# Performance work log

Measured on AMD Instinct MI355X. Metric: run time of the kernel, lower is better.

## Reference

```python
import jax, jax.numpy as jnp
import numpy as np


def _solve(f, lmbda, nu, repeats, l):
    h, w, nc = f.shape
    proj = l * (l + 1) // 2
    # enumeration order of (k1,k2) pairs matches the torch double loop
    k1s = np.array([k1 for k1 in range(l) for k2 in range(k1, l)], dtype=np.int32)
    k2s = np.array([k2 for k1 in range(l) for k2 in range(k1, l)], dtype=np.int32)
    zs = np.arange(l)
    # M[p, z] = 1 iff k1s[p] <= z <= k2s[p]  (the k_indices membership)
    M = jnp.asarray(((k1s[:, None] <= zs[None, :]) & (zs[None, :] <= k2s[:, None])).astype(np.float32))
    k1s_j = jnp.asarray(k1s)
    k2s_j = jnp.asarray(k2s)

    sigmap = 1.0 / (3.0 + l)
    sigmas = 1.0
    tauu = 1.0 / 6.0
    tau_mu = 1.0 / (2.0 + proj / 4.0)

    kl = jnp.arange(1, l + 1, dtype=jnp.float32) / l            # k/l, k=1..l
    dist2 = (kl[None, None, None, :] - f[..., None]) ** 2       # (h,w,nc,l)

    def bound(x1, x2):
        return 0.25 * (x1 * x1 + x2 * x2) - lmbda * dist2

    def parabola(p1, p2, p3, ubar, mu1, mu2):
        # forward differences, zero-padded at the far edge
        u1 = jnp.diff(ubar, axis=0, append=ubar[-1:, :, :, :])
        u2 = jnp.diff(ubar, axis=1, append=ubar[:, -1:, :, :])
        u3 = jnp.diff(ubar, axis=3, append=ubar[:, :, :, -1:])
        mu1sum = jnp.einsum('hwcp,pz->hwcz', mu1, M)
        mu2sum = jnp.einsum('hwcp,pz->hwcz', mu2, M)
        u1 = p1 + sigmap * (u1 + mu1sum)
        u2 = p2 + sigmap * (u2 + mu2sum)
        u3 = p3 + sigmap * u3
        B = bound(u1, u2)
        mask = u3 < B
        y = u3 + lmbda * dist2
        norm = jnp.sqrt(u1 * u1 + u2 * u2)
        a = 0.5 * norm                      # 2*0.25*norm
        b = (2.0 / 3.0) * (1.0 - 0.5 * y)   # 2/3*(1 - 2*0.25*y)
        neg_b = b < 0
        sb = jnp.sqrt(jnp.where(neg_b, -b, 1.0))   # sqrt(-b), guarded
        sb3 = sb * sb * sb
        d = jnp.where(neg_b, (a - sb3) * (a + sb3), a * a + b * b * b)
        d_pos = d >= 0
        c = jnp.cbrt(a + jnp.sqrt(jnp.where(d_pos, d, 0.0)))  # a+sqrt(d)>=0
        c_safe = jnp.where(c == 0, 1.0, c)
        ratio = jnp.clip(a / jnp.where(neg_b, sb3, 1.0), -1.0, 1.0)
        v_trig = 2.0 * sb * jnp.cos(jnp.arccos(ratio) / 3.0)
        v = jnp.where(d_pos & (c == 0), 0.0,
                      jnp.where(~d_pos, v_trig, c - b / c_safe))
        norm_safe = jnp.where(norm == 0, 1.0, norm)
        scale = (v / 0.5) / norm_safe       # v/(2*0.25)/norm
        p1n = jnp.where(mask, jnp.where(norm == 0, 0.0, scale * u1), u1)
        p2n = jnp.where(mask, jnp.where(norm == 0, 0.0, scale * u2), u2)
        p3n = jnp.where(mask, bound(p1n, p2n), u3)
        return p1n, p2n, p3n

    def l2proj(s1, s2, mb1, mb2):
        m1 = s1 - sigmas * mb1
        m2 = s2 - sigmas * mb2
        norm = jnp.sqrt(m1 * m1 + m2 * m2)
        mask = norm > nu
        ns = jnp.where(mask, norm, 1.0)
        return jnp.where(mask, m1 * nu / ns, m1), jnp.where(mask, m2 * nu / ns, m2)

    def mu_step(p1, p2, s1, s2, mu1, mu2):
        # interval sums sum_{k=k1..k2} p via exclusive cumsum differences
        zpad = jnp.zeros(p1.shape[:3] + (1,), p1.dtype)
        cs1 = jnp.concatenate([zpad, jnp.cumsum(p1, axis=3)], axis=3)
        cs2 = jnp.concatenate([zpad, jnp.cumsum(p2, axis=3)], axis=3)
        t1 = cs1[..., k2s_j + 1] - cs1[..., k1s_j]
        t2 = cs2[..., k2s_j + 1] - cs2[..., k1s_j]
        mu1n = mu1 + tau_mu * (s1 - t1)
        mu2n = mu2 + tau_mu * (s2 - t2)
        return mu1n, mu2n, 2.0 * mu1n - mu1, 2.0 * mu2n - mu2

    def clipping(p1, p2, p3, u):
        # adjoint (backward) differences of p[:-1] zero-padded on both sides
        z0 = jnp.zeros((1, w, nc, l), u.dtype)
        z1 = jnp.zeros((h, 1, nc, l), u.dtype)
        z3 = jnp.zeros((h, w, nc, 1), u.dtype)
        d1 = jnp.diff(jnp.concatenate([z0, p1[:-1], z0], axis=0), axis=0)
        d2 = jnp.diff(jnp.concatenate([z1, p2[:, :-1], z1], axis=1), axis=1)
        d3 = jnp.diff(jnp.concatenate([z3, p3[..., :-1], z3], axis=3), axis=3)
        un = jnp.clip(u + tauu * (d1 + d2 + d3), 0.0, 1.0)
        un = un.at[..., 0].set(1.0).at[..., l - 1].set(0.0)
        return un, 2.0 * un - u

    u0 = jnp.broadcast_to(f[..., None], (h, w, nc, l)).astype(jnp.float32)
    zl = jnp.zeros((h, w, nc, l), jnp.float32)
    zp = jnp.zeros((h, w, nc, proj), jnp.float32)
    state = (u0, u0, zl, zl, zl, zp, zp, zp, zp, zp, zp, jnp.array(False))

    def body(state, i):
        u, ubar, p1, p2, p3, s1, s2, mu1, mu2, mb1, mb2, done = state
        p1n, p2n, p3n = parabola(p1, p2, p3, ubar, mu1, mu2)
        s1n, s2n = l2proj(s1, s2, mb1, mb2)
        mu1n, mu2n, mb1n, mb2n = mu_step(p1n, p2n, s1n, s2n, mu1, mu2)
        un, ubarn = clipping(p1n, p2n, p3n, u)
        nrj = jnp.sum(jnp.abs(un - u))  # h_u vs h_un
        conv = ((i % 10) == 0) & (nrj / (w * h * l) <= 5e-5)
        keep = lambda old, new: jnp.where(done, old, new)
        new = (keep(u, un), keep(ubar, ubarn), keep(p1, p1n), keep(p2, p2n),
               keep(p3, p3n), keep(s1, s1n), keep(s2, s2n), keep(mu1, mu1n),
               keep(mu2, mu2n), keep(mb1, mb1n), keep(mb2, mb2n), done | conv)
        return new, None

    state, _ = jax.lax.scan(body, state, jnp.arange(repeats))
    return state[0]


def setup_inputs() -> dict:
    key = jax.random.key(0)
    f = jax.random.uniform(key, (384, 384, 1), dtype=jnp.float32)
    return {"f": f, "lmbda": jnp.float32(1.0), "nu": jnp.float32(1.0),
            "repeats": 6, "l": 12}


def reference(f, lmbda, nu, repeats, l):
    return _solve(f, lmbda, nu, repeats, l)
```

## Files before the change

kernel.cpp:

```cpp
#include <hip/hip_runtime.h>
#include <hip/hip_fp16.h>
#include <math.h>

#define H 384
#define W 384
#define NPIX (H * W)
#define L 12
#define REPEATS 6
#define LNP ((size_t)L * NPIX)

__host__ __device__ constexpr int pbase(int k1) { return k1 * L - (k1 * (k1 - 1)) / 2; }

struct alignas(8) P1 { __half2 mu, d; };

__device__ __forceinline__ void parabola_proj(float u1, float u2, float u3, float ld2,
                                              float& p1n, float& p2n, float& p3n) {
  const float n2 = u1 * u1 + u2 * u2;
  const float Bb = 0.25f * n2 - ld2;
  const bool mask = u3 < Bb;
  const float y = u3 + ld2;
  const float norm = sqrtf(n2);
  const float a = 0.5f * norm;
  const float b = (2.0f / 3.0f) * (1.0f - 0.5f * y);
  const bool neg_b = b < 0.0f;
  const float sb = sqrtf(neg_b ? -b : 1.0f);
  const float sb3 = sb * sb * sb;
  const float d = neg_b ? (a - sb3) * (a + sb3) : (a * a + b * b * b);
  const bool d_pos = d >= 0.0f;
  const float c = cbrtf(a + sqrtf(d_pos ? d : 0.0f));
  const float c_safe = (c == 0.0f) ? 1.0f : c;
  const float ratio = fminf(fmaxf(a / (neg_b ? sb3 : 1.0f), -1.0f), 1.0f);
  const float v_trig = 2.0f * sb * cosf(acosf(ratio) * (1.0f / 3.0f));
  const float v = (d_pos && c == 0.0f) ? 0.0f
                  : (!d_pos ? v_trig : (c - b / c_safe));
  const float norm_safe = (norm == 0.0f) ? 1.0f : norm;
  const float scale = (2.0f * v) / norm_safe;
  if (mask) {
    p1n = (norm == 0.0f) ? 0.0f : scale * u1;
    p2n = (norm == 0.0f) ? 0.0f : scale * u2;
    p3n = 0.25f * (p1n * p1n + p2n * p2n) - ld2;
  } else {
    p1n = u1; p2n = u2; p3n = u3;
  }
}

__device__ __forceinline__ void load_cs(int pix, const __half2* __restrict__ p12,
                                        float* cs1, float* cs2) {
  cs1[0] = 0.0f; cs2[0] = 0.0f;
#pragma unroll
  for (int z = 0; z < L; ++z) {
    const float2 t = __half22float2(p12[z * NPIX + pix]);
    cs1[z + 1] = cs1[z] + t.x;
    cs2[z + 1] = cs2[z] + t.y;
  }
}

__device__ __forceinline__ float2 pair_adv(float nu, float t1, float t2,
                                           __half2& mu, __half2& d) {
  const float2 dd = __half22float2(d);
  const float n2 = dd.x * dd.x + dd.y * dd.y;
  const float sc = fminf(nu * rsqrtf(n2), 1.0f);
  const float s1 = dd.x * sc, s2 = dd.y * sc;
  const float2 m = __half22float2(mu);
  const float tau = 1.0f / 21.5f;
  const float m1 = m.x + tau * (s1 - t1);
  const float m2 = m.y + tau * (s2 - t2);
  mu = __floats2half2_rn(m1, m2);
  d  = __floats2half2_rn(s1 - 2.0f * m1 + m.x, s2 - 2.0f * m2 + m.y);
  return make_float2(m1, m2);
}

template <int R, bool ACC>
__device__ __forceinline__ void row_step(float nu, const float* cs1, const float* cs2,
                                         P1* st, float* ms1, float* ms2) {
  float r1 = 0.0f, r2 = 0.0f;
#pragma unroll
  for (int k2 = L - 1; k2 >= R; --k2) {
    const float2 m = pair_adv(nu, cs1[k2 + 1] - cs1[R], cs2[k2 + 1] - cs2[R],
                              st[k2 - R].mu, st[k2 - R].d);
    if constexpr (ACC) { r1 += m.x; r2 += m.y; ms1[k2] += r1; ms2[k2] += r2; }
  }
}

template <int R, int N>
__device__ __forceinline__ void ck_io(int pix, P1* __restrict__ ck, P1* st, bool load) {
#pragma unroll
  for (int q = 0; q < N; ++q) {
    if (load) st[q] = ck[(pbase(R) + q) * NPIX + pix];
    else      ck[(pbase(R) + q) * NPIX + pix] = st[q];
  }
}

template <int KB, int KE, bool LOADCK, bool STORECK, int RA, int RB, int RC, int RD>
__device__ __forceinline__ void replay_worker(int pix, float nu,
    const __half2* __restrict__ hist, P1* __restrict__ ck,
    float* ms1, float* ms2, float* cs1, float* cs2) {
  constexpr int NA = 12 - RA;
  constexpr int NB = (RB < 12) ? 12 - RB : 1;
  constexpr int NC = (RC < 12) ? 12 - RC : 1;
  constexpr int ND = (RD < 12) ? 12 - RD : 1;
  P1 sa[NA], sb[NB], sc_[NC], sd[ND];
  if constexpr (LOADCK) {
    ck_io<RA, NA>(pix, ck, sa, true);
    if constexpr (RB < 12) ck_io<RB, NB>(pix, ck, sb, true);
    if constexpr (RC < 12) ck_io<RC, NC>(pix, ck, sc_, true);
    if constexpr (RD < 12) ck_io<RD, ND>(pix, ck, sd, true);
  } else {
    const __half2 z2 = __floats2half2_rn(0.0f, 0.0f);
#pragma unroll
    for (int q = 0; q < NA; ++q) { sa[q].mu = z2; sa[q].d = z2; }
#pragma unroll
    for (int q = 0; q < NB; ++q) { sb[q].mu = z2; sb[q].d = z2; }
#pragma unroll
    for (int q = 0; q < NC; ++q) { sc_[q].mu = z2; sc_[q].d = z2; }
#pragma unroll
    for (int q = 0; q < ND; ++q) { sd[q].mu = z2; sd[q].d = z2; }
  }

  for (int i = KB; i < KE - 1; ++i) {
    load_cs(pix, hist + (size_t)i * LNP, cs1, cs2);
    row_step<RA, false>(nu, cs1, cs2, sa, ms1, ms2);
    if constexpr (RB < 12) row_step<RB, false>(nu, cs1, cs2, sb, ms1, ms2);
    if constexpr (RC < 12) row_step<RC, false>(nu, cs1, cs2, sc_, ms1, ms2);
    if constexpr (RD < 12) row_step<RD, false>(nu, cs1, cs2, sd, ms1, ms2);
  }
  load_cs(pix, hist + (size_t)(KE - 1) * LNP, cs1, cs2);
  row_step<RA, true>(nu, cs1, cs2, sa, ms1, ms2);
  if constexpr (RB < 12) row_step<RB, true>(nu, cs1, cs2, sb, ms1, ms2);
  if constexpr (RC < 12) row_step<RC, true>(nu, cs1, cs2, sc_, ms1, ms2);
  if constexpr (RD < 12) row_step<RD, true>(nu, cs1, cs2, sd, ms1, ms2);
  if constexpr (STORECK) {
    ck_io<RA, NA>(pix, ck, sa, false);
    if constexpr (RB < 12) ck_io<RB, NB>(pix, ck, sb, false);
    if constexpr (RC < 12) ck_io<RC, NC>(pix, ck, sc_, false);
    if constexpr (RD < 12) ck_io<RD, ND>(pix, ck, sd, false);
  }
}

template <int WKR, bool FIRSTU, bool LAST>
__device__ __forceinline__ void epilogue(
    int pix, int lane, const float (*sms)[64][25],
    const float* cs1, const float* cs2, const float* __restrict__ f,
    const __half2* __restrict__ p12cur, const __half* __restrict__ p3,
    __half2* __restrict__ musum, __half* __restrict__ uh,
    float* __restrict__ uout, __half* __restrict__ ubar) {
  const int i = pix / W;
  const int j = pix - i * W;
  constexpr int z0 = 3 * WKR;
  float uold[3];
  if (FIRSTU) {
    const float fv = f[pix];
    uold[0] = fv; uold[1] = fv; uold[2] = fv;
  } else {
#pragma unroll
    for (int zz = 0; zz < 3; ++zz) uold[zz] = __half2float(uh[(z0 + zz) * NPIX + pix]);
  }
  float p3prev = (z0 == 0) ? 0.0f : __half2float(p3[(z0 - 1) * NPIX + pix]);
#pragma unroll
  for (int zz = 0; zz < 3; ++zz) {
    const int z = z0 + zz;
    if constexpr (!LAST) {
      float m1 = 0.0f, m2 = 0.0f;
#pragma unroll
      for (int w = 0; w < 4; ++w) {
        m1 += sms[w][lane][2 * z];
        m2 += sms[w][lane][2 * z + 1];
      }
      musum[z * NPIX + pix] = __floats2half2_rn(m1, m2);
    }
    const float p1o = cs1[z + 1] - cs1[z];
    const float p2o = cs2[z + 1] - cs2[z];
    const float p1up = (i > 0) ? __half22float2(p12cur[z * NPIX + pix - W]).x : 0.0f;
    const float p2lf = (j > 0) ? __half22float2(p12cur[z * NPIX + pix - 1]).y : 0.0f;
    const float d1 = ((i < H - 1) ? p1o : 0.0f) - p1up;
    const float d2 = ((j < W - 1) ? p2o : 0.0f) - p2lf;
    const float p3c = __half2float(p3[z * NPIX + pix]);
    const float d3 = ((z < L - 1) ? p3c : 0.0f) - p3prev;
    p3prev = p3c;
    float vn = fminf(fmaxf(uold[zz] + (1.0f / 6.0f) * (d1 + d2 + d3), 0.0f), 1.0f);
    if (z == 0) vn = 1.0f;
    if (z == L - 1) vn = 0.0f;
    if constexpr (LAST) {
      uout[pix * L + z] = vn;
    } else {
      uh[z * NPIX + pix] = __float2half(vn);
      ubar[z * NPIX + pix] = __float2half(2.0f * vn - uold[zz]);
    }
  }
}

template <int KB, int KE, bool LOADCK, bool STORECK, bool FIRSTU, bool LAST>
__global__ __launch_bounds__(256, 3) void k_dual(
    const float* __restrict__ nu_p, const float* __restrict__ f,
    const __half2* __restrict__ hist, P1* __restrict__ ck,
    const __half* __restrict__ p3, __half* __restrict__ uh,
    float* __restrict__ uout, __half2* __restrict__ musum,
    __half* __restrict__ ubar) {
  const int lane = threadIdx.x & 63;
  const int wkr  = threadIdx.x >> 6;
  const int pix  = blockIdx.x * 64 + lane;
  const float nu = *nu_p;
  constexpr int KCUR = KE - 1;

  __shared__ float sms[LAST ? 1 : 4][64][25];

  float cs1[L + 1], cs2[L + 1];
  if constexpr (!LAST) {
    float ms1[L], ms2[L];
#pragma unroll
    for (int z = 0; z < L; ++z) { ms1[z] = 0.0f; ms2[z] = 0.0f; }
    switch (wkr) {
      case 0: replay_worker<KB, KE, LOADCK, STORECK, 0, 4, 12, 12>(pix, nu, hist, ck, ms1, ms2, cs1, cs2); break;
      case 1: replay_worker<KB, KE, LOADCK, STORECK, 1, 5, 11, 12>(pix, nu, hist, ck, ms1, ms2, cs1, cs2); break;
      case 2: replay_worker<KB, KE, LOADCK, STORECK, 2, 6, 8, 12>(pix, nu, hist, ck, ms1, ms2, cs1, cs2); break;
      default:replay_worker<KB, KE, LOADCK, STORECK, 3, 7, 9, 10>(pix, nu, hist, ck, ms1, ms2, cs1, cs2); break;
    }
#pragma unroll
    for (int z = 0; z < L; ++z) {
      sms[wkr][lane][2 * z]     = ms1[z];
      sms[wkr][lane][2 * z + 1] = ms2[z];
    }
    __syncthreads();
  } else {
    load_cs(pix, hist + (size_t)KCUR * LNP, cs1, cs2);
  }

  const __half2* p12cur = hist + (size_t)KCUR * LNP;
  switch (wkr) {
    case 0: epilogue<0, FIRSTU, LAST>(pix, lane, sms, cs1, cs2, f, p12cur, p3, musum, uh, uout, ubar); break;
    case 1: epilogue<1, FIRSTU, LAST>(pix, lane, sms, cs1, cs2, f, p12cur, p3, musum, uh, uout, ubar); break;
    case 2: epilogue<2, FIRSTU, LAST>(pix, lane, sms, cs1, cs2, f, p12cur, p3, musum, uh, uout, ubar); break;
    default:epilogue<3, FIRSTU, LAST>(pix, lane, sms, cs1, cs2, f, p12cur, p3, musum, uh, uout, ubar); break;
  }
}

template <bool FIRST>
__global__ __launch_bounds__(256) void k_parabola(
    const float* __restrict__ f, const float* __restrict__ lam_p,
    const __half* __restrict__ ubar, const __half2* __restrict__ musum,
    const __half2* __restrict__ p12prev, __half2* __restrict__ p12cur,
    __half* __restrict__ p3) {
  const int pix = blockIdx.x * 256 + threadIdx.x;
  const int z = blockIdx.y;
  const int idx = z * NPIX + pix;
  const int i = pix / W;
  const int j = pix - i * W;
  const float lam = *lam_p;
  const float fv = f[pix];
  const float sigmap = 1.0f / 15.0f;

  float u1, u2, u3;
  if (FIRST) {
    const float du1 = (i < H - 1) ? (f[pix + W] - fv) : 0.0f;
    const float du2 = (j < W - 1) ? (f[pix + 1] - fv) : 0.0f;
    u1 = sigmap * du1; u2 = sigmap * du2; u3 = 0.0f;
  } else {
    const float ub = __half2float(ubar[idx]);
    const float du1 = (i < H - 1) ? (__half2float(ubar[idx + W]) - ub) : 0.0f;
    const float du2 = (j < W - 1) ? (__half2float(ubar[idx + 1]) - ub) : 0.0f;
    const float du3 = (z < L - 1) ? (__half2float(ubar[idx + NPIX]) - ub) : 0.0f;
    const float2 ms = __half22float2(musum[idx]);
    const float2 pp = __half22float2(p12prev[idx]);
    const float p3v = __half2float(p3[idx]);
    u1 = pp.x + sigmap * (du1 + ms.x);
    u2 = pp.y + sigmap * (du2 + ms.y);
    u3 = p3v + sigmap * du3;
  }
  const float kl = (float)(z + 1) * (1.0f / (float)L);
  const float fd = kl - fv;
  const float ld2 = lam * (fd * fd);
  float p1n, p2n, p3n;
  parabola_proj(u1, u2, u3, ld2, p1n, p2n, p3n);
  p12cur[idx] = __floats2half2_rn(p1n, p2n);
  p3[idx] = __float2half(p3n);
}

extern "C" void kernel_launch(void* const* d_in, const int* in_sizes, int n_in,
                              void* d_out, int out_size, void* d_ws, size_t ws_size,
                              hipStream_t stream) {
  const float* f   = (const float*)d_in[0];
  const float* lam = (const float*)d_in[1];
  const float* nu  = (const float*)d_in[2];
  float* u = (float*)d_out;

  char* base = (char*)d_ws;
  size_t off = 0;
  auto carve = [&](size_t bytes) -> void* {
    void* p = base + off;
    off += (bytes + 255) & ~size_t(255);
    return p;
  };
  __half2* hist  = (__half2*)carve(sizeof(__half2) * (size_t)REPEATS * LNP);
  P1*      ck    = (P1*)carve(sizeof(P1) * (size_t)78 * NPIX);
  __half2* musum = (__half2*)carve(sizeof(__half2) * LNP);
  __half*  p3    = (__half*)carve(sizeof(__half) * LNP);
  __half*  ubar  = (__half*)carve(sizeof(__half) * LNP);
  __half*  uh    = (__half*)carve(sizeof(__half) * LNP);

  const dim3 gA(NPIX / 256, L);
  const int gB = NPIX / 64;

  k_parabola<true><<<gA, 256, 0, stream>>>(f, lam, ubar, musum, hist, hist, p3);
  k_dual<0, 1, false, false, true, false><<<gB, 256, 0, stream>>>(nu, f, hist, ck, p3, uh, u, musum, ubar);
  k_parabola<false><<<gA, 256, 0, stream>>>(f, lam, ubar, musum, hist + 0 * LNP, hist + 1 * LNP, p3);
  k_dual<0, 2, false, false, false, false><<<gB, 256, 0, stream>>>(nu, f, hist, ck, p3, uh, u, musum, ubar);
  k_parabola<false><<<gA, 256, 0, stream>>>(f, lam, ubar, musum, hist + 1 * LNP, hist + 2 * LNP, p3);
  k_dual<0, 3, false, true, false, false><<<gB, 256, 0, stream>>>(nu, f, hist, ck, p3, uh, u, musum, ubar);
  k_parabola<false><<<gA, 256, 0, stream>>>(f, lam, ubar, musum, hist + 2 * LNP, hist + 3 * LNP, p3);
  k_dual<3, 4, true, false, false, false><<<gB, 256, 0, stream>>>(nu, f, hist, ck, p3, uh, u, musum, ubar);
  k_parabola<false><<<gA, 256, 0, stream>>>(f, lam, ubar, musum, hist + 3 * LNP, hist + 4 * LNP, p3);
  k_dual<3, 5, true, false, false, false><<<gB, 256, 0, stream>>>(nu, f, hist, ck, p3, uh, u, musum, ubar);
  k_parabola<false><<<gA, 256, 0, stream>>>(f, lam, ubar, musum, hist + 4 * LNP, hist + 5 * LNP, p3);
  k_dual<5, 6, false, false, false, true><<<gB, 256, 0, stream>>>(nu, f, hist, ck, p3, uh, u, musum, ubar);
}
```

Baseline: 225.0 us.

## Replace first dual iteration replay with closed-form mu/d state from zero init

The first iteration of the pairwise mu update starts from zero state, so the shrink step gives s=0 and mu = -tau*t. The code now computes that state in closed form. The first k_dual computes the per-z mu sums directly from prefix and suffix sums of cs. Later replays seed their state from that closed form instead of replaying iteration 0, which removes one full replay step and the shared-memory reduction in the first kernel. It relies on the zero-init assumption, and the half-precision state is now produced by a different arithmetic path.

```diff
diff --git a/kernel.cpp b/kernel.cpp
--- a/kernel.cpp
+++ b/kernel.cpp
@@ -70,6 +70,18 @@
   return make_float2(m1, m2);
 }
 
+template <int R>
+__device__ __forceinline__ void row_init0(const float* cs01, const float* cs02, P1* st) {
+  const float tau = 1.0f / 21.5f;
+#pragma unroll
+  for (int k2 = R; k2 < L; ++k2) {
+    const float m1 = -(tau * (cs01[k2 + 1] - cs01[R]));
+    const float m2 = -(tau * (cs02[k2 + 1] - cs02[R]));
+    st[k2 - R].mu = __floats2half2_rn(m1, m2);
+    st[k2 - R].d  = __floats2half2_rn(-2.0f * m1, -2.0f * m2);
+  }
+}
+
 template <int R, bool ACC>
 __device__ __forceinline__ void row_step(float nu, const float* cs1, const float* cs2,
                                          P1* st, float* ms1, float* ms2) {
@@ -91,10 +103,15 @@
   }
 }
 
-template <int KB, int KE, bool LOADCK, bool STORECK, int RA, int RB, int RC, int RD>
+template <int MODE, int RA, int RB, int RC, int RD>
 __device__ __forceinline__ void replay_worker(int pix, float nu,
     const __half2* __restrict__ hist, P1* __restrict__ ck,
     float* ms1, float* ms2, float* cs1, float* cs2) {
+  constexpr bool INIT0  = (MODE == 1 || MODE == 2);
+  constexpr bool LOADCK = (MODE == 3 || MODE == 4);
+  constexpr bool STORECK = (MODE == 2);
+  constexpr int KB = INIT0 ? 1 : 3;
+  constexpr int KE = MODE + 1;
   constexpr int NA = 12 - RA;
   constexpr int NB = (RB < 12) ? 12 - RB : 1;
   constexpr int NC = (RC < 12) ? 12 - RC : 1;
@@ -106,15 +123,11 @@
     if constexpr (RC < 12) ck_io<RC, NC>(pix, ck, sc_, true);
     if constexpr (RD < 12) ck_io<RD, ND>(pix, ck, sd, true);
   } else {
-    const __half2 z2 = __floats2half2_rn(0.0f, 0.0f);
-#pragma unroll
-    for (int q = 0; q < NA; ++q) { sa[q].mu = z2; sa[q].d = z2; }
-#pragma unroll
-    for (int q = 0; q < NB; ++q) { sb[q].mu = z2; sb[q].d = z2; }
-#pragma unroll
-    for (int q = 0; q < NC; ++q) { sc_[q].mu = z2; sc_[q].d = z2; }
-#pragma unroll
-    for (int q = 0; q < ND; ++q) { sd[q].mu = z2; sd[q].d = z2; }
+    load_cs(pix, hist, cs1, cs2);
+    row_init0<RA>(cs1, cs2, sa);
+    if constexpr (RB < 12) row_init0<RB>(cs1, cs2, sb);
+    if constexpr (RC < 12) row_init0<RC>(cs1, cs2, sc_);
+    if constexpr (RD < 12) row_init0<RD>(cs1, cs2, sd);
   }
 
   for (int i = KB; i < KE - 1; ++i) {
@@ -137,9 +150,44 @@
   }
 }
 
+template <int WKR>
+__device__ __forceinline__ void cf0_ms(const float* cs1, const float* cs2,
+                                       float* mr1, float* mr2) {
+  float p1a[L], p2a[L], s1a[L], s2a[L];
+  float a1 = 0.0f, a2 = 0.0f;
+#pragma unroll
+  for (int z = 0; z < L; ++z) { a1 += cs1[z]; p1a[z] = a1; a2 += cs2[z]; p2a[z] = a2; }
+  a1 = 0.0f; a2 = 0.0f;
+#pragma unroll
+  for (int z = L - 1; z >= 0; --z) { a1 += cs1[z + 1]; s1a[z] = a1; a2 += cs2[z + 1]; s2a[z] = a2; }
+  const float tau = 1.0f / 21.5f;
+#pragma unroll
+  for (int zz = 0; zz < 3; ++zz) {
+    const int z = 3 * WKR + zz;
+    mr1[zz] = -tau * ((float)(z + 1) * s1a[z] - (float)(L - z) * p1a[z]);
+    mr2[zz] = -tau * ((float)(z + 1) * s2a[z] - (float)(L - z) * p2a[z]);
+  }
+}
+
+template <int WKR>
+__device__ __forceinline__ void reduce_ms(const float (*sms)[64][25], int lane,
+                                          float* mr1, float* mr2) {
+#pragma unroll
+  for (int zz = 0; zz < 3; ++zz) {
+    const int z = 3 * WKR + zz;
+    float m1 = 0.0f, m2 = 0.0f;
+#pragma unroll
+    for (int w = 0; w < 4; ++w) {
+      m1 += sms[w][lane][2 * z];
+      m2 += sms[w][lane][2 * z + 1];
+    }
+    mr1[zz] = m1; mr2[zz] = m2;
+  }
+}
+
 template <int WKR, bool FIRSTU, bool LAST>
 __device__ __forceinline__ void epilogue(
-    int pix, int lane, const float (*sms)[64][25],
+    int pix, const float* mr1, const float* mr2,
     const float* cs1, const float* cs2, const float* __restrict__ f,
     const __half2* __restrict__ p12cur, const __half* __restrict__ p3,
     __half2* __restrict__ musum, __half* __restrict__ uh,
@@ -160,13 +208,7 @@
   for (int zz = 0; zz < 3; ++zz) {
     const int z = z0 + zz;
     if constexpr (!LAST) {
-      float m1 = 0.0f, m2 = 0.0f;
-#pragma unroll
-      for (int w = 0; w < 4; ++w) {
-        m1 += sms[w][lane][2 * z];
-        m2 += sms[w][lane][2 * z + 1];
-      }
-      musum[z * NPIX + pix] = __floats2half2_rn(m1, m2);
+      musum[z * NPIX + pix] = __floats2half2_rn(mr1[zz], mr2[zz]);
     }
     const float p1o = cs1[z + 1] - cs1[z];
     const float p2o = cs2[z + 1] - cs2[z];
@@ -189,7 +231,7 @@
   }
 }
 
-template <int KB, int KE, bool LOADCK, bool STORECK, bool FIRSTU, bool LAST>
+template <int MODE>
 __global__ __launch_bounds__(256, 3) void k_dual(
     const float* __restrict__ nu_p, const float* __restrict__ f,
     const __half2* __restrict__ hist, P1* __restrict__ ck,
@@ -200,20 +242,33 @@
   const int wkr  = threadIdx.x >> 6;
   const int pix  = blockIdx.x * 64 + lane;
   const float nu = *nu_p;
-  constexpr int KCUR = KE - 1;
-
-  __shared__ float sms[LAST ? 1 : 4][64][25];
+  constexpr int KCUR = MODE;
+  constexpr bool HASSMS = (MODE >= 1 && MODE <= 4);
+
+  __shared__ float sms[HASSMS ? 4 : 1][64][25];
 
   float cs1[L + 1], cs2[L + 1];
-  if constexpr (!LAST) {
+  float mred1[3], mred2[3];
+
+  if constexpr (MODE == 0) {
+    load_cs(pix, hist, cs1, cs2);
+    switch (wkr) {
+      case 0: cf0_ms<0>(cs1, cs2, mred1, mred2); break;
+      case 1: cf0_ms<1>(cs1, cs2, mred1, mred2); break;
+      case 2: cf0_ms<2>(cs1, cs2, mred1, mred2); break;
+      default:cf0_ms<3>(cs1, cs2, mred1, mred2); break;
+    }
+  } else if constexpr (MODE == 5) {
+    load_cs(pix, hist + (size_t)KCUR * LNP, cs1, cs2);
+  } else {
     float ms1[L], ms2[L];
 #pragma unroll
     for (int z = 0; z < L; ++z) { ms1[z] = 0.0f; ms2[z] = 0.0f; }
     switch (wkr) {
-      case 0: replay_worker<KB, KE, LOADCK, STORECK, 0, 4, 12, 12>(pix, nu, hist, ck, ms1, ms2, cs1, cs2); break;
-      case 1: replay_worker<KB, KE, LOADCK, STORECK, 1, 5, 11, 12>(pix, nu, hist, ck, ms1, ms2, cs1, cs2); break;
-      case 2: replay_worker<KB, KE, LOADCK, STORECK, 2, 6, 8, 12>(pix, nu, hist, ck, ms1, ms2, cs1, cs2); break;
-      default:replay_worker<KB, KE, LOADCK, STORECK, 3, 7, 9, 10>(pix, nu, hist, ck, ms1, ms2, cs1, cs2); break;
+      case 0: replay_worker<MODE, 0, 4, 12, 12>(pix, nu, hist, ck, ms1, ms2, cs1, cs2); break;
+      case 1: replay_worker<MODE, 1, 5, 11, 12>(pix, nu, hist, ck, ms1, ms2, cs1, cs2); break;
+      case 2: replay_worker<MODE, 2, 6, 8, 12>(pix, nu, hist, ck, ms1, ms2, cs1, cs2); break;
+      default:replay_worker<MODE, 3, 7, 9, 10>(pix, nu, hist, ck, ms1, ms2, cs1, cs2); break;
     }
 #pragma unroll
     for (int z = 0; z < L; ++z) {
@@ -221,16 +276,22 @@
       sms[wkr][lane][2 * z + 1] = ms2[z];
     }
     __syncthreads();
-  } else {
-    load_cs(pix, hist + (size_t)KCUR * LNP, cs1, cs2);
+    switch (wkr) {
+      case 0: reduce_ms<0>(sms, lane, mred1, mred2); break;
+      case 1: reduce_ms<1>(sms, lane, mred1, mred2); break;
+      case 2: reduce_ms<2>(sms, lane, mred1, mred2); break;
+      default:reduce_ms<3>(sms, lane, mred1, mred2); break;
+    }
   }
 
   const __half2* p12cur = hist + (size_t)KCUR * LNP;
+  constexpr bool FIRSTU = (MODE == 0);
+  constexpr bool LAST = (MODE == 5);
   switch (wkr) {
-    case 0: epilogue<0, FIRSTU, LAST>(pix, lane, sms, cs1, cs2, f, p12cur, p3, musum, uh, uout, ubar); break;
-    case 1: epilogue<1, FIRSTU, LAST>(pix, lane, sms, cs1, cs2, f, p12cur, p3, musum, uh, uout, ubar); break;
-    case 2: epilogue<2, FIRSTU, LAST>(pix, lane, sms, cs1, cs2, f, p12cur, p3, musum, uh, uout, ubar); break;
-    default:epilogue<3, FIRSTU, LAST>(pix, lane, sms, cs1, cs2, f, p12cur, p3, musum, uh, uout, ubar); break;
+    case 0: epilogue<0, FIRSTU, LAST>(pix, mred1, mred2, cs1, cs2, f, p12cur, p3, musum, uh, uout, ubar); break;
+    case 1: epilogue<1, FIRSTU, LAST>(pix, mred1, mred2, cs1, cs2, f, p12cur, p3, musum, uh, uout, ubar); break;
+    case 2: epilogue<2, FIRSTU, LAST>(pix, mred1, mred2, cs1, cs2, f, p12cur, p3, musum, uh, uout, ubar); break;
+    default:epilogue<3, FIRSTU, LAST>(pix, mred1, mred2, cs1, cs2, f, p12cur, p3, musum, uh, uout, ubar); break;
   }
 }
 
@@ -301,15 +362,15 @@
   const int gB = NPIX / 64;
 
   k_parabola<true><<<gA, 256, 0, stream>>>(f, lam, ubar, musum, hist, hist, p3);
-  k_dual<0, 1, false, false, true, false><<<gB, 256, 0, stream>>>(nu, f, hist, ck, p3, uh, u, musum, ubar);
+  k_dual<0><<<gB, 256, 0, stream>>>(nu, f, hist, ck, p3, uh, u, musum, ubar);
   k_parabola<false><<<gA, 256, 0, stream>>>(f, lam, ubar, musum, hist + 0 * LNP, hist + 1 * LNP, p3);
-  k_dual<0, 2, false, false, false, false><<<gB, 256, 0, stream>>>(nu, f, hist, ck, p3, uh, u, musum, ubar);
+  k_dual<1><<<gB, 256, 0, stream>>>(nu, f, hist, ck, p3, uh, u, musum, ubar);
   k_parabola<false><<<gA, 256, 0, stream>>>(f, lam, ubar, musum, hist + 1 * LNP, hist + 2 * LNP, p3);
-  k_dual<0, 3, false, true, false, false><<<gB, 256, 0, stream>>>(nu, f, hist, ck, p3, uh, u, musum, ubar);
+  k_dual<2><<<gB, 256, 0, stream>>>(nu, f, hist, ck, p3, uh, u, musum, ubar);
   k_parabola<false><<<gA, 256, 0, stream>>>(f, lam, ubar, musum, hist + 2 * LNP, hist + 3 * LNP, p3);
-  k_dual<3, 4, true, false, false, false><<<gB, 256, 0, stream>>>(nu, f, hist, ck, p3, uh, u, musum, ubar);
+  k_dual<3><<<gB, 256, 0, stream>>>(nu, f, hist, ck, p3, uh, u, musum, ubar);
   k_parabola<false><<<gA, 256, 0, stream>>>(f, lam, ubar, musum, hist + 3 * LNP, hist + 4 * LNP, p3);
-  k_dual<3, 5, true, false, false, false><<<gB, 256, 0, stream>>>(nu, f, hist, ck, p3, uh, u, musum, ubar);
+  k_dual<4><<<gB, 256, 0, stream>>>(nu, f, hist, ck, p3, uh, u, musum, ubar);
   k_parabola<false><<<gA, 256, 0, stream>>>(f, lam, ubar, musum, hist + 4 * LNP, hist + 5 * LNP, p3);
-  k_dual<5, 6, false, false, false, true><<<gB, 256, 0, stream>>>(nu, f, hist, ck, p3, uh, u, musum, ubar);
-}
+  k_dual<5><<<gB, 256, 0, stream>>>(nu, f, hist, ck, p3, uh, u, musum, ubar);
+}
```

After: 242.2 us. +7.6%, slower.
